# Kernel tuning notes

Measured on AMD Instinct MI355X. Metric: run time of the kernel, lower is better.

## Reference

```python
import jax, jax.numpy as jnp
import numpy as np

N_NODES = 50000
N_EDGES = 800000
VOCAB = 32000
IN_FEATS = 128
N_HIDDEN = 128
N_CLASSES = 40
SEQ_LEN = 20
PAD_IX = 0


def setup_inputs() -> dict:
    key = jax.random.key(0)
    ks = jax.random.split(key, 6)
    features = jax.random.randint(ks[0], (N_NODES, SEQ_LEN), 0, VOCAB, dtype=jnp.int64 if jax.config.jax_enable_x64 else jnp.int32).astype(jnp.int32)
    src = jax.random.randint(ks[1], (N_EDGES,), 0, N_NODES, dtype=jnp.int32)
    dst = jax.random.randint(ks[2], (N_EDGES,), 0, N_NODES, dtype=jnp.int32)
    emb_weight = jax.random.normal(ks[3], (VOCAB, IN_FEATS), dtype=jnp.float32) * 0.02
    emb_weight = emb_weight.at[PAD_IX].set(0.0)  # padding_idx row is zero
    W1 = jax.random.normal(ks[4], (IN_FEATS, N_HIDDEN), dtype=jnp.float32) * (1.0 / np.sqrt(IN_FEATS))
    b1 = jnp.zeros((N_HIDDEN,), dtype=jnp.float32)
    W2 = jax.random.normal(ks[5], (N_HIDDEN, N_CLASSES), dtype=jnp.float32) * (1.0 / np.sqrt(N_HIDDEN))
    b2 = jnp.zeros((N_CLASSES,), dtype=jnp.float32)
    return {"features": features, "src": src, "dst": dst, "emb_weight": emb_weight,
            "W1": W1, "b1": b1, "W2": W2, "b2": b2}


def _graph_conv(h, src, dst, W, b, n_nodes, activation=None):
    # DGL GraphConv with norm='both': D_out^{-1/2} applied to src feats,
    # sum-aggregate along edges, D_in^{-1/2} on dst, then linear (+bias, act).
    ones = jnp.ones(src.shape[0], dtype=h.dtype)
    out_deg = jax.ops.segment_sum(ones, src, num_segments=n_nodes)
    in_deg = jax.ops.segment_sum(ones, dst, num_segments=n_nodes)
    h = h * jax.lax.rsqrt(jnp.maximum(out_deg, 1.0))[:, None]
    agg = jax.ops.segment_sum(h[src], dst, num_segments=n_nodes)  # gather + scatter-add (SpMM)
    agg = agg * jax.lax.rsqrt(jnp.maximum(in_deg, 1.0))[:, None]
    out = agg @ W + b
    if activation is not None:
        out = activation(out)
    return out


def reference(features, src, dst, emb_weight, W1, b1, W2, b2):
    n_nodes = features.shape[0]
    # embedding mean-pool over non-pad tokens: [n_nodes, seq, d] -> [n_nodes, d]
    seq_len = jnp.maximum(jnp.sum(features != PAD_IX, axis=1, keepdims=True), 1).astype(emb_weight.dtype)
    h = jnp.take(emb_weight, features, axis=0).sum(axis=1) / seq_len
    h = _graph_conv(h, src, dst, W1, b1, n_nodes, activation=jax.nn.relu)
    # dropout is identity in eval mode
    h = _graph_conv(h, src, dst, W2, b2, n_nodes)
    return h
```

## Files before the change

### kernel.cpp

```cpp
#include <hip/hip_runtime.h>
#include <math.h>

#define N_NODES 50000
#define N_EDGES 800000
#define IN_FEATS 128
#define N_HIDDEN 128
#define N_CLASSES 40
#define SEQ_LEN 20
#define VOCAB 32000
#define BUCKET_CAP 64

#define NPART 196
#define PCAP 4608
#define SCAT_BLOCKS 392
#define POOL_BLOCKS 12500
#define SCATPOOL_BLOCKS (SCAT_BLOCKS + POOL_BLOCKS)

#define PREP_BLOCKS 89
#define EGEMM_BLOCKS 500
#define GEMM2_BLOCKS 782
#define SCALE_BLOCKS 12500

typedef __attribute__((ext_vector_type(8))) short bf16x8;
typedef __attribute__((ext_vector_type(4))) float f32x4;

#define AS1 __attribute__((address_space(1)))
#define AS3 __attribute__((address_space(3)))

__device__ __forceinline__ void gld_lds4(const void* g, void* l) {
    __builtin_amdgcn_global_load_lds((const AS1 unsigned int*)g,
                                     (AS3 unsigned int*)l, 4, 0, 0);
}
__device__ __forceinline__ void vm_wait0() {
    asm volatile("s_waitcnt vmcnt(0)" ::: "memory");
}

__device__ inline unsigned short f2bf(float x) {
    union { float f; unsigned int u; } v; v.f = x;
    unsigned int r = v.u + 0x7FFF + ((v.u >> 16) & 1);
    return (unsigned short)(r >> 16);
}
__device__ inline float bf2f(unsigned short b) {
    union { float f; unsigned int u; } v; v.u = ((unsigned int)b) << 16;
    return v.f;
}


__global__ __launch_bounds__(256) void prep_kernel(
        int4* __restrict__ pcnt_zero, const float* __restrict__ W1,
        unsigned short* __restrict__ W1p, const float* __restrict__ W2,
        unsigned short* __restrict__ W2p) {
    int b = blockIdx.x;
    int t = threadIdx.x;
    if (b == 0) {
        if (t < 128) pcnt_zero[t] = make_int4(0, 0, 0, 0);
    } else if (b < 65) {
        int i = (b - 1) * 256 + t;
        int tile = i >> 9, rem = i & 511;
        int ln = rem >> 3, j = rem & 7;
        int nt = tile >> 2, kb = tile & 3;
        int k = kb * 32 + ((ln >> 4) << 3) + j;
        int n = nt * 16 + (ln & 15);
        W1p[i] = f2bf(W1[k * 128 + n]);
    } else {
        int i = (b - 65) * 256 + t;
        int tile = i >> 9, rem = i & 511;
        int ln = rem >> 3, j = rem & 7;
        int nt = tile >> 2, kb = tile & 3;
        int k = kb * 32 + ((ln >> 4) << 3) + j;
        int n = nt * 16 + (ln & 15);
        W2p[i] = (n < N_CLASSES) ? f2bf(W2[k * N_CLASSES + n]) : (unsigned short)0;
    }
}

__global__ __launch_bounds__(256) void egemm_kernel(
        const float* __restrict__ emb, const unsigned short* __restrict__ W1p,
        unsigned short* __restrict__ Ep) {
    const int wave = threadIdx.x >> 6, lane = threadIdx.x & 63;
    const int quad = lane >> 4, m = lane & 15;
    const int row0 = blockIdx.x * 64 + wave * 16;
    const int arow = row0 + m;
    const float4* ap = (const float4*)(emb + arow * 128 + quad * 8);
    bf16x8 a[4];
    #pragma unroll
    for (int kb = 0; kb < 4; ++kb) {
        float4 x = ap[kb * 8];
        float4 y = ap[kb * 8 + 1];
        bf16x8 t;
        t[0] = f2bf(x.x); t[1] = f2bf(x.y); t[2] = f2bf(x.z); t[3] = f2bf(x.w);
        t[4] = f2bf(y.x); t[5] = f2bf(y.y); t[6] = f2bf(y.z); t[7] = f2bf(y.w);
        a[kb] = t;
    }
    const int rbase = row0 + quad * 4;
    #pragma unroll
    for (int nt = 0; nt < 8; ++nt) {
        const unsigned short* wp = W1p + (nt * 4) * 512 + lane * 8;
        bf16x8 b0 = *(const bf16x8*)(wp + 0 * 512);
        bf16x8 b1 = *(const bf16x8*)(wp + 1 * 512);
        bf16x8 b2 = *(const bf16x8*)(wp + 2 * 512);
        bf16x8 b3 = *(const bf16x8*)(wp + 3 * 512);
        f32x4 acc = {0.f, 0.f, 0.f, 0.f};
        acc = __builtin_amdgcn_mfma_f32_16x16x32_bf16(a[0], b0, acc, 0, 0, 0);
        acc = __builtin_amdgcn_mfma_f32_16x16x32_bf16(a[1], b1, acc, 0, 0, 0);
        acc = __builtin_amdgcn_mfma_f32_16x16x32_bf16(a[2], b2, acc, 0, 0, 0);
        acc = __builtin_amdgcn_mfma_f32_16x16x32_bf16(a[3], b3, acc, 0, 0, 0);
        #pragma unroll
        for (int r = 0; r < 4; ++r)
            Ep[(rbase + r) * 128 + nt * 16 + m] = f2bf(acc[r]);
    }
}

__global__ __launch_bounds__(256) void scatpool_kernel(
        const int* __restrict__ src, const int* __restrict__ dst,
        unsigned int* __restrict__ pcnt_s, unsigned char* __restrict__ pbuf_s,
        unsigned int* __restrict__ pcnt_d, unsigned int* __restrict__ pbuf_d,
        const int* __restrict__ feats, const unsigned short* __restrict__ Ep,
        unsigned short* __restrict__ G1) {
    __shared__ unsigned int shm[5120];
    int b = blockIdx.x;
    int t = threadIdx.x;
    if (b < 196) {
        unsigned int* lhist = shm;
        unsigned int* lbase = shm + 256;
        for (int i = t; i < NPART; i += 256) lhist[i] = 0u;
        __syncthreads();
        int base = b * 4096;
        int pid[16]; unsigned int rank[16]; unsigned char val[16];
        #pragma unroll
        for (int k = 0; k < 16; ++k) {
            int i = base + k * 256 + t;
            pid[k] = -1;
            if (i < N_EDGES) {
                int u = src[i];
                val[k] = (unsigned char)(u & 255);
                pid[k] = u >> 8;
                rank[k] = atomicAdd(&lhist[pid[k]], 1u);
            }
        }
        __syncthreads();
        for (int i = t; i < NPART; i += 256)
            lbase[i] = atomicAdd(&pcnt_s[i], lhist[i]);
        __syncthreads();
        #pragma unroll
        for (int k = 0; k < 16; ++k) {
            if (pid[k] >= 0) {
                unsigned int pos = lbase[pid[k]] + rank[k];
                if (pos < PCAP) pbuf_s[pid[k] * PCAP + pos] = val[k];
            }
        }
    } else if (b < 392) {
        unsigned int* lhist = shm;
        unsigned int* lbase = shm + 256;
        for (int i = t; i < NPART; i += 256) lhist[i] = 0u;
        __syncthreads();
        int base = (b - 196) * 4096;
        int pid[16]; unsigned int rank[16]; unsigned int val[16];
        #pragma unroll
        for (int k = 0; k < 16; ++k) {
            int i = base + k * 256 + t;
            pid[k] = -1;
            if (i < N_EDGES) {
                int u = src[i];
                int d = dst[i];
                val[k] = ((unsigned int)u << 8) | (unsigned int)(d & 255);
                pid[k] = d >> 8;
                rank[k] = atomicAdd(&lhist[pid[k]], 1u);
            }
        }
        __syncthreads();
        for (int i = t; i < NPART; i += 256)
            lbase[i] = atomicAdd(&pcnt_d[i], lhist[i]);
        __syncthreads();
        #pragma unroll
        for (int k = 0; k < 16; ++k) {
            if (pid[k] >= 0) {
                unsigned int pos = lbase[pid[k]] + rank[k];
                if (pos < PCAP) pbuf_d[pid[k] * PCAP + pos] = val[k];
            }
        }
    } else {
        unsigned int (*pstage)[SEQ_LEN][64] = (unsigned int (*)[SEQ_LEN][64])shm;
        int pb = b - 392;
        int w = t >> 6;
        int v = pb * 4 + w;
        int lane = t & 63;

        int toks[SEQ_LEN];
        const int4* tk4 = (const int4*)(feats + v * SEQ_LEN);
        #pragma unroll
        for (int q = 0; q < SEQ_LEN / 4; ++q) {
            int4 tt = tk4[q];
            toks[4 * q + 0] = tt.x;
            toks[4 * q + 1] = tt.y;
            toks[4 * q + 2] = tt.z;
            toks[4 * q + 3] = tt.w;
        }
        int nz = 0;
        #pragma unroll
        for (int s = 0; s < SEQ_LEN; ++s) nz += (toks[s] != 0);

        #pragma unroll
        for (int s = 0; s < SEQ_LEN; ++s)
            gld_lds4(Ep + toks[s] * 128 + lane * 2, &pstage[w][s][0]);
        vm_wait0();
        float a0 = 0.f, a1 = 0.f;
        #pragma unroll
        for (int s = 0; s < SEQ_LEN; ++s) {
            unsigned int x = pstage[w][s][lane];
            a0 += bf2f((unsigned short)(x & 0xffffu));
            a1 += bf2f((unsigned short)(x >> 16));
        }
        float sc = 1.f / (float)max(nz, 1);
        ushort2 o = {f2bf(a0 * sc), f2bf(a1 * sc)};
        ((ushort2*)G1)[v * 64 + lane] = o;
    }
}

__global__ __launch_bounds__(256) void count_kernel(
        const unsigned int* __restrict__ pcnt_s, const unsigned char* __restrict__ pbuf_s,
        const unsigned int* __restrict__ pcnt_d, const unsigned int* __restrict__ pbuf_d,
        unsigned int* __restrict__ cnt, float* __restrict__ routf,
        unsigned short* __restrict__ bucketu) {
    __shared__ unsigned int ho[256];
    __shared__ unsigned int hi_[256];
    int p = blockIdx.x, t = threadIdx.x;
    ho[t] = 0u;
    hi_[t] = 0u;
    __syncthreads();
    int ns = min((int)pcnt_s[p], PCAP);
    const unsigned char* ps = pbuf_s + p * PCAP;
    for (int i = t; i < ns; i += 256) atomicAdd(&ho[ps[i]], 1u);
    int nd = min((int)pcnt_d[p], PCAP);
    const unsigned int* pd = pbuf_d + p * PCAP;
    for (int i = t; i < nd; i += 256) {
        unsigned int e = pd[i];
        unsigned int d = e & 255u;
        unsigned int slot = atomicAdd(&hi_[d], 1u);
        if (slot < BUCKET_CAP)
            bucketu[(p * 256 + (int)d) * BUCKET_CAP + slot] = (unsigned short)(e >> 8);
    }
    __syncthreads();
    int v = p * 256 + t;
    if (v < N_NODES) {
        cnt[v] = (ho[t] << 16) | (hi_[t] & 0xffffu);
        routf[v] = rsqrtf(fmaxf((float)ho[t], 1.f));
    }
}

__global__ __launch_bounds__(256) void scale_g1_kernel(
        const float* __restrict__ routf, unsigned int* __restrict__ G1u) {
    int i = blockIdx.x * 256 + threadIdx.x;
    int row = i >> 6;
    float ro = routf[row];
    unsigned int x = G1u[i];
    unsigned short lo = f2bf(bf2f((unsigned short)(x & 0xffffu)) * ro);
    unsigned short hi = f2bf(bf2f((unsigned short)(x >> 16)) * ro);
    G1u[i] = (unsigned int)lo | ((unsigned int)hi << 16);
}

__global__ __launch_bounds__(256) void spmm1_kernel(
        const unsigned int* __restrict__ cnt, const float* __restrict__ routf,
        const unsigned short* __restrict__ bucketu, const unsigned short* __restrict__ G,
        const float* __restrict__ b1, unsigned short* __restrict__ h1) {
    __shared__ unsigned short idxs[256];
    __shared__ unsigned int stg[4][16][64];
    int t = threadIdx.x;
    int node = t >> 6, lane = t & 63;
    int v = blockIdx.x * 4 + node;
    idxs[t] = bucketu[blockIdx.x * 256 + t];
    int ind = (int)(cnt[v] & 0xffffu);
    float rov = routf[v];
    float2 bb = ((const float2*)b1)[lane];
    int n = min(ind, BUCKET_CAP);
    const unsigned short* bk = &idxs[node * BUCKET_CAP];
    float a0 = 0.f, a1 = 0.f;
    for (int base = 0; base < n; base += 16) {
        int m = min(16, n - base);
        #pragma unroll 4
        for (int j = 0; j < m; ++j)
            gld_lds4(G + bk[base + j] * 128 + lane * 2, &stg[node][j][0]);
        vm_wait0();
        #pragma unroll 4
        for (int j = 0; j < m; ++j) {
            unsigned int x = stg[node][j][lane];
            a0 += bf2f((unsigned short)(x & 0xffffu));
            a1 += bf2f((unsigned short)(x >> 16));
        }
    }
    float rin = rsqrtf(fmaxf((float)ind, 1.f));
    float v0 = fmaxf(a0 * rin + bb.x, 0.f) * rov;
    float v1 = fmaxf(a1 * rin + bb.y, 0.f) * rov;
    ushort2 o = {f2bf(v0), f2bf(v1)};
    ((ushort2*)h1)[v * 64 + lane] = o;
}

__global__ __launch_bounds__(256) void gemm2_kernel(
        const unsigned short* __restrict__ h1, const unsigned short* __restrict__ W2p,
        unsigned short* __restrict__ G2) {
    const int wave = threadIdx.x >> 6, lane = threadIdx.x & 63;
    const int quad = lane >> 4, m = lane & 15;
    const int row0 = blockIdx.x * 64 + wave * 16;
    const int arow = min(row0 + m, N_NODES - 1);
    const unsigned short* ap = h1 + arow * 128 + quad * 8;
    bf16x8 a0 = *(const bf16x8*)(ap + 0);
    bf16x8 a1 = *(const bf16x8*)(ap + 32);
    bf16x8 a2 = *(const bf16x8*)(ap + 64);
    bf16x8 a3 = *(const bf16x8*)(ap + 96);
    const int rbase = row0 + quad * 4;
    #pragma unroll
    for (int nt = 0; nt < 3; ++nt) {
        const unsigned short* wp = W2p + (nt * 4) * 512 + lane * 8;
        bf16x8 b0 = *(const bf16x8*)(wp + 0 * 512);
        bf16x8 b1 = *(const bf16x8*)(wp + 1 * 512);
        bf16x8 b2 = *(const bf16x8*)(wp + 2 * 512);
        bf16x8 b3 = *(const bf16x8*)(wp + 3 * 512);
        f32x4 acc = {0.f, 0.f, 0.f, 0.f};
        acc = __builtin_amdgcn_mfma_f32_16x16x32_bf16(a0, b0, acc, 0, 0, 0);
        acc = __builtin_amdgcn_mfma_f32_16x16x32_bf16(a1, b1, acc, 0, 0, 0);
        acc = __builtin_amdgcn_mfma_f32_16x16x32_bf16(a2, b2, acc, 0, 0, 0);
        acc = __builtin_amdgcn_mfma_f32_16x16x32_bf16(a3, b3, acc, 0, 0, 0);
        int col = nt * 16 + m;
        #pragma unroll
        for (int r = 0; r < 4; ++r) {
            int row = rbase + r;
            if (row < N_NODES && col < N_CLASSES)
                G2[row * 64 + col] = f2bf(acc[r]);
        }
    }
}

__global__ __launch_bounds__(256) void spmm2_kernel(
        const unsigned int* __restrict__ cnt, const unsigned short* __restrict__ bucketu,
        const unsigned short* __restrict__ G2, const float* __restrict__ b2,
        float* __restrict__ out) {
    __shared__ unsigned short idxs[256];
    __shared__ unsigned short stg[4][16][64];
    int t = threadIdx.x;
    int node = t >> 6, f = t & 63;
    int v = blockIdx.x * 4 + node;
    idxs[t] = bucketu[blockIdx.x * 256 + t];
    int ind = (int)(cnt[v] & 0xffffu);
    int n = min(ind, BUCKET_CAP);
    const unsigned short* bk = &idxs[node * BUCKET_CAP];
    int half = f >> 5, sub = f & 31;
    float acc = 0.f;
    for (int base = 0; base < n; base += 16) {
        int m = min(16, n - base);
        #pragma unroll 2
        for (int j = 0; j < m; j += 2) {
            int u0 = bk[base + j];
            int u1 = (j + 1 < m) ? bk[base + j + 1] : u0;
            int u = half ? u1 : u0;
            gld_lds4(G2 + u * 64 + sub * 2, &stg[node][j][0]);
        }
        vm_wait0();
        if (f < N_CLASSES) {
            #pragma unroll 4
            for (int j = 0; j < m; ++j) acc += bf2f(stg[node][j][f]);
        }
    }
    if (f < N_CLASSES) {
        float rin = rsqrtf(fmaxf((float)ind, 1.f));
        out[v * N_CLASSES + f] = acc * rin + b2[f];
    }
}

extern "C" void kernel_launch(void* const* d_in, const int* in_sizes, int n_in,
                              void* d_out, int out_size, void* d_ws, size_t ws_size,
                              hipStream_t stream) {
    const int*   feats = (const int*)d_in[0];
    const int*   src   = (const int*)d_in[1];
    const int*   dst   = (const int*)d_in[2];
    const float* emb   = (const float*)d_in[3];
    const float* W1    = (const float*)d_in[4];
    const float* b1    = (const float*)d_in[5];
    const float* W2    = (const float*)d_in[6];
    const float* b2    = (const float*)d_in[7];
    float* out = (float*)d_out;

    char* w = (char*)d_ws;
    unsigned int*   cnt     = (unsigned int*)(w + 0);
    unsigned int*   pcnt_s  = (unsigned int*)(w + 200704);
    unsigned int*   pcnt_d  = (unsigned int*)(w + 201728);
    float*          routf   = (float*)(w + 202752);
    unsigned short* bucketu = (unsigned short*)(w + 403456);
    unsigned char*  pbuf_s  = (unsigned char*)(w + 6803456);
    unsigned int*   pbuf_d  = (unsigned int*)(w + 7706624);
    unsigned short* Ep      = (unsigned short*)(w + 11319296);
    unsigned short* h1      = (unsigned short*)(w + 6803456);
    unsigned short* G1      = (unsigned short*)(w + 19603456);
    unsigned short* G2      = (unsigned short*)(w + 32403456);
    unsigned short* W1p     = (unsigned short*)(w + 38803456);
    unsigned short* W2p     = (unsigned short*)(w + 38836224);

    prep_kernel<<<PREP_BLOCKS, 256, 0, stream>>>(
        (int4*)pcnt_s, W1, W1p, W2, W2p);
    egemm_kernel<<<EGEMM_BLOCKS, 256, 0, stream>>>(emb, W1p, Ep);
    scatpool_kernel<<<SCATPOOL_BLOCKS, 256, 0, stream>>>(
        src, dst, pcnt_s, pbuf_s, pcnt_d, pbuf_d, feats, Ep, G1);
    count_kernel<<<NPART, 256, 0, stream>>>(
        pcnt_s, pbuf_s, pcnt_d, pbuf_d, cnt, routf, bucketu);
    scale_g1_kernel<<<SCALE_BLOCKS, 256, 0, stream>>>(routf, (unsigned int*)G1);
    spmm1_kernel<<<POOL_BLOCKS, 256, 0, stream>>>(cnt, routf, bucketu, G1, b1, h1);
    gemm2_kernel<<<GEMM2_BLOCKS, 256, 0, stream>>>(h1, W2p, G2);
    spmm2_kernel<<<POOL_BLOCKS, 256, 0, stream>>>(cnt, bucketu, G2, b2, out);
}
```

Baseline: 200.8 us.

## Fuse embedding GEMM with edge scatter, fold out-degree scale into pool, widen gathers

The embedding GEMM now runs as extra blocks of the edge-partition scatter kernel instead of as its own launch. Token pooling moves to its own kernel after the degree count so the out-degree normalisation is folded in, which removes the separate scale kernel and its extra pass over G1. The row gathers in pooling, spmm1 and spmm2 switch from 4-byte to 16-byte global-to-LDS loads with 32-row staging, cutting the number of load instructions. The cost is one extra pool launch and larger LDS staging buffers in the SpMM kernels.

```diff
diff --git a/kernel.cpp b/kernel.cpp
--- a/kernel.cpp
+++ b/kernel.cpp
@@ -12,14 +12,10 @@
 
 #define NPART 196
 #define PCAP 4608
-#define SCAT_BLOCKS 392
+#define EGS_BLOCKS 892
 #define POOL_BLOCKS 12500
-#define SCATPOOL_BLOCKS (SCAT_BLOCKS + POOL_BLOCKS)
-
 #define PREP_BLOCKS 89
-#define EGEMM_BLOCKS 500
 #define GEMM2_BLOCKS 782
-#define SCALE_BLOCKS 12500
 
 typedef __attribute__((ext_vector_type(8))) short bf16x8;
 typedef __attribute__((ext_vector_type(4))) float f32x4;
@@ -27,9 +23,9 @@
 #define AS1 __attribute__((address_space(1)))
 #define AS3 __attribute__((address_space(3)))
 
-__device__ __forceinline__ void gld_lds4(const void* g, void* l) {
+__device__ __forceinline__ void gld_lds16(const void* g, void* l) {
     __builtin_amdgcn_global_load_lds((const AS1 unsigned int*)g,
-                                     (AS3 unsigned int*)l, 4, 0, 0);
+                                     (AS3 unsigned int*)l, 16, 0, 0);
 }
 __device__ __forceinline__ void vm_wait0() {
     asm volatile("s_waitcnt vmcnt(0)" ::: "memory");
@@ -73,50 +69,13 @@
     }
 }
 
-__global__ __launch_bounds__(256) void egemm_kernel(
-        const float* __restrict__ emb, const unsigned short* __restrict__ W1p,
-        unsigned short* __restrict__ Ep) {
-    const int wave = threadIdx.x >> 6, lane = threadIdx.x & 63;
-    const int quad = lane >> 4, m = lane & 15;
-    const int row0 = blockIdx.x * 64 + wave * 16;
-    const int arow = row0 + m;
-    const float4* ap = (const float4*)(emb + arow * 128 + quad * 8);
-    bf16x8 a[4];
-    #pragma unroll
-    for (int kb = 0; kb < 4; ++kb) {
-        float4 x = ap[kb * 8];
-        float4 y = ap[kb * 8 + 1];
-        bf16x8 t;
-        t[0] = f2bf(x.x); t[1] = f2bf(x.y); t[2] = f2bf(x.z); t[3] = f2bf(x.w);
-        t[4] = f2bf(y.x); t[5] = f2bf(y.y); t[6] = f2bf(y.z); t[7] = f2bf(y.w);
-        a[kb] = t;
-    }
-    const int rbase = row0 + quad * 4;
-    #pragma unroll
-    for (int nt = 0; nt < 8; ++nt) {
-        const unsigned short* wp = W1p + (nt * 4) * 512 + lane * 8;
-        bf16x8 b0 = *(const bf16x8*)(wp + 0 * 512);
-        bf16x8 b1 = *(const bf16x8*)(wp + 1 * 512);
-        bf16x8 b2 = *(const bf16x8*)(wp + 2 * 512);
-        bf16x8 b3 = *(const bf16x8*)(wp + 3 * 512);
-        f32x4 acc = {0.f, 0.f, 0.f, 0.f};
-        acc = __builtin_amdgcn_mfma_f32_16x16x32_bf16(a[0], b0, acc, 0, 0, 0);
-        acc = __builtin_amdgcn_mfma_f32_16x16x32_bf16(a[1], b1, acc, 0, 0, 0);
-        acc = __builtin_amdgcn_mfma_f32_16x16x32_bf16(a[2], b2, acc, 0, 0, 0);
-        acc = __builtin_amdgcn_mfma_f32_16x16x32_bf16(a[3], b3, acc, 0, 0, 0);
-        #pragma unroll
-        for (int r = 0; r < 4; ++r)
-            Ep[(rbase + r) * 128 + nt * 16 + m] = f2bf(acc[r]);
-    }
-}
-
-__global__ __launch_bounds__(256) void scatpool_kernel(
+__global__ __launch_bounds__(256) void egemm_scat_kernel(
         const int* __restrict__ src, const int* __restrict__ dst,
         unsigned int* __restrict__ pcnt_s, unsigned char* __restrict__ pbuf_s,
         unsigned int* __restrict__ pcnt_d, unsigned int* __restrict__ pbuf_d,
-        const int* __restrict__ feats, const unsigned short* __restrict__ Ep,
-        unsigned short* __restrict__ G1) {
-    __shared__ unsigned int shm[5120];
+        const float* __restrict__ emb, const unsigned short* __restrict__ W1p,
+        unsigned short* __restrict__ Ep) {
+    __shared__ unsigned int shm[512];
     int b = blockIdx.x;
     int t = threadIdx.x;
     if (b < 196) {
@@ -179,40 +138,38 @@
             }
         }
     } else {
-        unsigned int (*pstage)[SEQ_LEN][64] = (unsigned int (*)[SEQ_LEN][64])shm;
-        int pb = b - 392;
-        int w = t >> 6;
-        int v = pb * 4 + w;
-        int lane = t & 63;
-
-        int toks[SEQ_LEN];
-        const int4* tk4 = (const int4*)(feats + v * SEQ_LEN);
-        #pragma unroll
-        for (int q = 0; q < SEQ_LEN / 4; ++q) {
-            int4 tt = tk4[q];
-            toks[4 * q + 0] = tt.x;
-            toks[4 * q + 1] = tt.y;
-            toks[4 * q + 2] = tt.z;
-            toks[4 * q + 3] = tt.w;
-        }
-        int nz = 0;
-        #pragma unroll
-        for (int s = 0; s < SEQ_LEN; ++s) nz += (toks[s] != 0);
-
-        #pragma unroll
-        for (int s = 0; s < SEQ_LEN; ++s)
-            gld_lds4(Ep + toks[s] * 128 + lane * 2, &pstage[w][s][0]);
-        vm_wait0();
-        float a0 = 0.f, a1 = 0.f;
-        #pragma unroll
-        for (int s = 0; s < SEQ_LEN; ++s) {
-            unsigned int x = pstage[w][s][lane];
-            a0 += bf2f((unsigned short)(x & 0xffffu));
-            a1 += bf2f((unsigned short)(x >> 16));
-        }
-        float sc = 1.f / (float)max(nz, 1);
-        ushort2 o = {f2bf(a0 * sc), f2bf(a1 * sc)};
-        ((ushort2*)G1)[v * 64 + lane] = o;
+        const int wave = t >> 6, lane = t & 63;
+        const int quad = lane >> 4, m = lane & 15;
+        const int row0 = (b - 392) * 64 + wave * 16;
+        const int arow = row0 + m;
+        const float4* ap = (const float4*)(emb + arow * 128 + quad * 8);
+        bf16x8 a[4];
+        #pragma unroll
+        for (int kb = 0; kb < 4; ++kb) {
+            float4 x = ap[kb * 8];
+            float4 y = ap[kb * 8 + 1];
+            bf16x8 tt;
+            tt[0] = f2bf(x.x); tt[1] = f2bf(x.y); tt[2] = f2bf(x.z); tt[3] = f2bf(x.w);
+            tt[4] = f2bf(y.x); tt[5] = f2bf(y.y); tt[6] = f2bf(y.z); tt[7] = f2bf(y.w);
+            a[kb] = tt;
+        }
+        const int rbase = row0 + quad * 4;
+        #pragma unroll
+        for (int nt = 0; nt < 8; ++nt) {
+            const unsigned short* wp = W1p + (nt * 4) * 512 + lane * 8;
+            bf16x8 b0 = *(const bf16x8*)(wp + 0 * 512);
+            bf16x8 b1 = *(const bf16x8*)(wp + 1 * 512);
+            bf16x8 b2 = *(const bf16x8*)(wp + 2 * 512);
+            bf16x8 b3 = *(const bf16x8*)(wp + 3 * 512);
+            f32x4 acc = {0.f, 0.f, 0.f, 0.f};
+            acc = __builtin_amdgcn_mfma_f32_16x16x32_bf16(a[0], b0, acc, 0, 0, 0);
+            acc = __builtin_amdgcn_mfma_f32_16x16x32_bf16(a[1], b1, acc, 0, 0, 0);
+            acc = __builtin_amdgcn_mfma_f32_16x16x32_bf16(a[2], b2, acc, 0, 0, 0);
+            acc = __builtin_amdgcn_mfma_f32_16x16x32_bf16(a[3], b3, acc, 0, 0, 0);
+            #pragma unroll
+            for (int r = 0; r < 4; ++r)
+                Ep[(rbase + r) * 128 + nt * 16 + m] = f2bf(acc[r]);
+        }
     }
 }
 
@@ -247,15 +204,38 @@
     }
 }
 
-__global__ __launch_bounds__(256) void scale_g1_kernel(
-        const float* __restrict__ routf, unsigned int* __restrict__ G1u) {
-    int i = blockIdx.x * 256 + threadIdx.x;
-    int row = i >> 6;
-    float ro = routf[row];
-    unsigned int x = G1u[i];
-    unsigned short lo = f2bf(bf2f((unsigned short)(x & 0xffffu)) * ro);
-    unsigned short hi = f2bf(bf2f((unsigned short)(x >> 16)) * ro);
-    G1u[i] = (unsigned int)lo | ((unsigned int)hi << 16);
+__global__ __launch_bounds__(256) void pool_kernel(
+        const float* __restrict__ routf, const int* __restrict__ feats,
+        const unsigned short* __restrict__ Ep, unsigned short* __restrict__ G1) {
+    __shared__ unsigned int pstage[4][SEQ_LEN][64];
+    __shared__ int tokl[4][SEQ_LEN];
+    int t = threadIdx.x;
+    int w = t >> 6, lane = t & 63;
+    int v = blockIdx.x * 4 + w;
+    int mytok = 0;
+    if (lane < SEQ_LEN) {
+        mytok = feats[v * SEQ_LEN + lane];
+        tokl[w][lane] = mytok;
+    }
+    int nz = (int)__popcll(__ballot(lane < SEQ_LEN && mytok != 0));
+    __syncthreads();
+    #pragma unroll
+    for (int g = 0; g < SEQ_LEN / 4; ++g) {
+        int tok = tokl[w][4 * g + (lane >> 4)];
+        gld_lds16(Ep + tok * 128 + (lane & 15) * 8, &pstage[w][4 * g][0]);
+    }
+    float ro = routf[v];
+    vm_wait0();
+    float a0 = 0.f, a1 = 0.f;
+    #pragma unroll
+    for (int s = 0; s < SEQ_LEN; ++s) {
+        unsigned int x = pstage[w][s][lane];
+        a0 += bf2f((unsigned short)(x & 0xffffu));
+        a1 += bf2f((unsigned short)(x >> 16));
+    }
+    float sc = ro / (float)max(nz, 1);
+    ushort2 o = {f2bf(a0 * sc), f2bf(a1 * sc)};
+    ((ushort2*)G1)[v * 64 + lane] = o;
 }
 
 __global__ __launch_bounds__(256) void spmm1_kernel(
@@ -263,7 +243,7 @@
         const unsigned short* __restrict__ bucketu, const unsigned short* __restrict__ G,
         const float* __restrict__ b1, unsigned short* __restrict__ h1) {
     __shared__ unsigned short idxs[256];
-    __shared__ unsigned int stg[4][16][64];
+    __shared__ unsigned int stg[4][32][64];
     int t = threadIdx.x;
     int node = t >> 6, lane = t & 63;
     int v = blockIdx.x * 4 + node;
@@ -272,13 +252,15 @@
     float rov = routf[v];
     float2 bb = ((const float2*)b1)[lane];
     int n = min(ind, BUCKET_CAP);
-    const unsigned short* bk = &idxs[node * BUCKET_CAP];
     float a0 = 0.f, a1 = 0.f;
-    for (int base = 0; base < n; base += 16) {
-        int m = min(16, n - base);
-        #pragma unroll 4
-        for (int j = 0; j < m; ++j)
-            gld_lds4(G + bk[base + j] * 128 + lane * 2, &stg[node][j][0]);
+    for (int base = 0; base < n; base += 32) {
+        int m = min(32, n - base);
+        int nin = (m + 3) >> 2;
+        for (int g = 0; g < nin; ++g) {
+            int rc = min(base + 4 * g + (lane >> 4), n - 1);
+            int u = idxs[node * 64 + rc];
+            gld_lds16(G + u * 128 + (lane & 15) * 8, &stg[node][4 * g][0]);
+        }
         vm_wait0();
         #pragma unroll 4
         for (int j = 0; j < m; ++j) {
@@ -334,24 +316,21 @@
         const unsigned short* __restrict__ G2, const float* __restrict__ b2,
         float* __restrict__ out) {
     __shared__ unsigned short idxs[256];
-    __shared__ unsigned short stg[4][16][64];
+    __shared__ unsigned short stg[4][32][64];
     int t = threadIdx.x;
     int node = t >> 6, f = t & 63;
     int v = blockIdx.x * 4 + node;
     idxs[t] = bucketu[blockIdx.x * 256 + t];
     int ind = (int)(cnt[v] & 0xffffu);
     int n = min(ind, BUCKET_CAP);
-    const unsigned short* bk = &idxs[node * BUCKET_CAP];
-    int half = f >> 5, sub = f & 31;
     float acc = 0.f;
-    for (int base = 0; base < n; base += 16) {
-        int m = min(16, n - base);
-        #pragma unroll 2
-        for (int j = 0; j < m; j += 2) {
-            int u0 = bk[base + j];
-            int u1 = (j + 1 < m) ? bk[base + j + 1] : u0;
-            int u = half ? u1 : u0;
-            gld_lds4(G2 + u * 64 + sub * 2, &stg[node][j][0]);
+    for (int base = 0; base < n; base += 32) {
+        int m = min(32, n - base);
+        int nin = (m + 7) >> 3;
+        for (int g = 0; g < nin; ++g) {
+            int rc = min(base + 8 * g + (f >> 3), n - 1);
+            int u = idxs[node * 64 + rc];
+            gld_lds16(G2 + u * 64 + (f & 7) * 8, &stg[node][8 * g][0]);
         }
         vm_wait0();
         if (f < N_CLASSES) {
@@ -393,14 +372,12 @@
     unsigned short* W1p     = (unsigned short*)(w + 38803456);
     unsigned short* W2p     = (unsigned short*)(w + 38836224);
 
-    prep_kernel<<<PREP_BLOCKS, 256, 0, stream>>>(
-        (int4*)pcnt_s, W1, W1p, W2, W2p);
-    egemm_kernel<<<EGEMM_BLOCKS, 256, 0, stream>>>(emb, W1p, Ep);
-    scatpool_kernel<<<SCATPOOL_BLOCKS, 256, 0, stream>>>(
-        src, dst, pcnt_s, pbuf_s, pcnt_d, pbuf_d, feats, Ep, G1);
+    prep_kernel<<<PREP_BLOCKS, 256, 0, stream>>>((int4*)pcnt_s, W1, W1p, W2, W2p);
+    egemm_scat_kernel<<<EGS_BLOCKS, 256, 0, stream>>>(
+        src, dst, pcnt_s, pbuf_s, pcnt_d, pbuf_d, emb, W1p, Ep);
     count_kernel<<<NPART, 256, 0, stream>>>(
         pcnt_s, pbuf_s, pcnt_d, pbuf_d, cnt, routf, bucketu);
-    scale_g1_kernel<<<SCALE_BLOCKS, 256, 0, stream>>>(routf, (unsigned int*)G1);
+    pool_kernel<<<POOL_BLOCKS, 256, 0, stream>>>(routf, feats, Ep, G1);
     spmm1_kernel<<<POOL_BLOCKS, 256, 0, stream>>>(cnt, routf, bucketu, G1, b1, h1);
     gemm2_kernel<<<GEMM2_BLOCKS, 256, 0, stream>>>(h1, W2p, G2);
     spmm2_kernel<<<POOL_BLOCKS, 256, 0, stream>>>(cnt, bucketu, G2, b2, out);
```

New measurement: 190.8 us. -5.0%, faster.
